# Kernel tuning notes

Measured on AMD Instinct MI355X. Metric: run time of the kernel, lower is better.

Reference implementation:

```python
import jax, jax.numpy as jnp
import numpy as np

LATENT_DIM = 32
INPUT_DIM = 16
N_UNITS = 20
N_TRAJ = 4096
T = 512


def setup_inputs() -> dict:
    key = jax.random.key(0)
    ks = jax.random.split(key, 8)
    cat_dim = LATENT_DIM + INPUT_DIM
    s1 = 1.0 / np.sqrt(cat_dim)
    s2 = 1.0 / np.sqrt(N_UNITS)
    return {
        "data": jax.random.normal(ks[0], (N_TRAJ, T, INPUT_DIM), dtype=jnp.float32),
        "time_steps": jnp.arange(T, dtype=jnp.float32),
        "Wu1": jax.random.normal(ks[1], (cat_dim, N_UNITS), dtype=jnp.float32) * s1,
        "bu1": jnp.zeros((N_UNITS,), dtype=jnp.float32),
        "Wu2": jax.random.normal(ks[2], (N_UNITS, LATENT_DIM), dtype=jnp.float32) * s2,
        "bu2": jnp.zeros((LATENT_DIM,), dtype=jnp.float32),
        "Wr1": jax.random.normal(ks[3], (cat_dim, N_UNITS), dtype=jnp.float32) * s1,
        "br1": jnp.zeros((N_UNITS,), dtype=jnp.float32),
        "Wr2": jax.random.normal(ks[4], (N_UNITS, LATENT_DIM), dtype=jnp.float32) * s2,
        "br2": jnp.zeros((LATENT_DIM,), dtype=jnp.float32),
        "Wn1": jax.random.normal(ks[5], (cat_dim, N_UNITS), dtype=jnp.float32) * s1,
        "bn1": jnp.zeros((N_UNITS,), dtype=jnp.float32),
        "Wn2": jax.random.normal(ks[6], (N_UNITS, LATENT_DIM), dtype=jnp.float32) * s2,
        "bn2": jnp.zeros((LATENT_DIM,), dtype=jnp.float32),
    }


def _mlp(h, W1, b1, W2, b2):
    # 2-layer MLP with tanh hidden, linear out
    return jnp.tanh(h @ W1 + b1) @ W2 + b2


def reference(data, time_steps, Wu1, bu1, Wu2, bu2, Wr1, br1, Wr2, br2, Wn1, bn1, Wn2, bn2):
    n_traj = data.shape[0]
    latent_dim = Wu2.shape[1]

    def step(prev_y, xi):
        yc = jnp.concatenate([prev_y, xi], axis=-1)            # [B, L+D]
        u = jax.nn.sigmoid(_mlp(yc, Wu1, bu1, Wu2, bu2))       # update gate
        r = jax.nn.sigmoid(_mlp(yc, Wr1, br1, Wr2, br2))       # reset gate
        cc = jnp.concatenate([prev_y * r, xi], axis=-1)
        n = jnp.tanh(_mlp(cc, Wn1, bn1, Wn2, bn2))             # candidate state
        new_y = (1.0 - u) * n + u * prev_y
        return new_y, new_y

    prev_y = jnp.zeros((n_traj, latent_dim), dtype=data.dtype)
    xs = jnp.swapaxes(data, 0, 1)                              # [T, B, D]
    yi, ys = jax.lax.scan(step, prev_y, xs)
    latent_ys = jnp.swapaxes(ys, 0, 1)                         # [B, T, L]
    return yi, latent_ys
```

## Files before the change

### kernel.cpp

```cpp
#include <hip/hip_runtime.h>

#define T_STEPS 512
#define NTRAJ   4096
#define LAT     32
#define INPD    16
#define HID     20
#define CAT     48

__device__ __forceinline__ float fast_tanh(float x) {
    float e = __expf(2.0f * x);
    float r = __builtin_amdgcn_rcpf(e + 1.0f);
    return fmaf(-2.0f, r, 1.0f);
}
__device__ __forceinline__ float fast_sigmoid(float x) {
    float e = __expf(-x);
    return __builtin_amdgcn_rcpf(e + 1.0f);
}

template<int I> __device__ __forceinline__ float ror16(float v) {
    if constexpr (I == 0) {
        return v;
    } else {
        int r = __builtin_amdgcn_update_dpp(0, __float_as_int(v),
                                            0x120 | I, 0xF, 0xF, true);
        return __int_as_float(r);
    }
}

#define REP16(M) M(0) M(1) M(2) M(3) M(4) M(5) M(6) M(7) \
                 M(8) M(9) M(10) M(11) M(12) M(13) M(14) M(15)

__global__ __launch_bounds__(256, 2) void rnn_fused(
    const float* __restrict__ data,
    const float* __restrict__ Wu1, const float* __restrict__ bu1,
    const float* __restrict__ Wu2, const float* __restrict__ bu2,
    const float* __restrict__ Wr1, const float* __restrict__ br1,
    const float* __restrict__ Wr2, const float* __restrict__ br2,
    const float* __restrict__ Wn1, const float* __restrict__ bn1,
    const float* __restrict__ Wn2, const float* __restrict__ bn2,
    float* __restrict__ out_yi, float* __restrict__ out_lat)
{
    const int tid  = threadIdx.x;
    const int w    = tid >> 6;
    const int lane = tid & 63;
    const int c    = lane & 31;
    const int g    = lane >> 5;
    const int p    = (lane >> 4) & 1;
    const int b    = (blockIdx.x << 2) + w;

    const float* W1 = g ? Wr1 : Wu1;
    const float* B1 = g ? br1 : bu1;
    const float* W2 = g ? Wr2 : Wu2;
    const float* B2 = g ? br2 : bu2;
    const bool realc = (c < HID);

    float wa_a[16], wa_b[16], wa_x[16], wb_a[16], wb_b[16];
    float wc_a[16], wc_b[16], wc_x[16], wd_a[16], wd_b[16];
    #pragma unroll
    for (int i = 0; i < 16; ++i) {
        int s  = (c - i) & 15;
        int sa = 16 * p + s;
        int sb = 16 * (1 - p) + s;
        int sx = 32 + s;
        wa_a[i] = realc ? W1[sa * HID + c] : 0.0f;
        wa_b[i] = realc ? W1[sb * HID + c] : 0.0f;
        wa_x[i] = realc ? W1[sx * HID + c] : 0.0f;
        wb_a[i] = (sa < HID) ? W2[sa * LAT + c] : 0.0f;
        wb_b[i] = (sb < HID) ? W2[sb * LAT + c] : 0.0f;
        wc_a[i] = realc ? Wn1[sa * HID + c] : 0.0f;
        wc_b[i] = realc ? Wn1[sb * HID + c] : 0.0f;
        wc_x[i] = realc ? Wn1[sx * HID + c] : 0.0f;
        wd_a[i] = (sa < HID) ? Wn2[sa * LAT + c] : 0.0f;
        wd_b[i] = (sb < HID) ? Wn2[sb * LAT + c] : 0.0f;
    }
    const float ba = realc ? B1[c] : 0.0f;
    const float bb = B2[c];
    const float bc = realc ? bn1[c] : 0.0f;
    const float bd = bn2[c];

    const float* xptr = data + (size_t)b * T_STEPS * INPD + (lane & 15);
    float x0 = xptr[0];
    float x1 = xptr[INPD];

    float y  = 0.0f;
    float y2 = 0.0f;
    float* olat = out_lat + (size_t)b * T_STEPS * LAT + c;

    for (int t = 0; t < T_STEPS; ++t) {
        int tf = t + 2; tf = (tf < T_STEPS) ? tf : (T_STEPS - 1);
        float xn = xptr[(size_t)tf * INPD];

        float acc[4] = {ba, 0.f, 0.f, 0.f};
        #define PA(i) \
            acc[(i)&3]     = fmaf(ror16<(i)>(y),  wa_a[(i)], acc[(i)&3]); \
            acc[((i)+1)&3] = fmaf(ror16<(i)>(y2), wa_b[(i)], acc[((i)+1)&3]); \
            acc[((i)+2)&3] = fmaf(ror16<(i)>(x0), wa_x[(i)], acc[((i)+2)&3]);
        REP16(PA)
        #undef PA
        float h1 = fast_tanh((acc[0] + acc[1]) + (acc[2] + acc[3]));
        float h2 = __shfl_xor(h1, 16);

        float bcc[4] = {bb, 0.f, 0.f, 0.f};
        #define PB(i) \
            bcc[(i)&3]     = fmaf(ror16<(i)>(h1), wb_a[(i)], bcc[(i)&3]); \
            bcc[((i)+1)&3] = fmaf(ror16<(i)>(h2), wb_b[(i)], bcc[((i)+1)&3]);
        REP16(PB)
        #undef PB
        float gate = fast_sigmoid((bcc[0] + bcc[1]) + (bcc[2] + bcc[3]));

        float exch  = __shfl_xor(gate, 32);
        float u_all = g ? exch : gate;
        float r_all = g ? gate : exch;
        float ry    = r_all * y;
        float ry2   = __shfl_xor(ry, 16);

        float ccc[4] = {bc, 0.f, 0.f, 0.f};
        #define PC(i) \
            ccc[(i)&3]     = fmaf(ror16<(i)>(ry),  wc_a[(i)], ccc[(i)&3]); \
            ccc[((i)+1)&3] = fmaf(ror16<(i)>(ry2), wc_b[(i)], ccc[((i)+1)&3]); \
            ccc[((i)+2)&3] = fmaf(ror16<(i)>(x0),  wc_x[(i)], ccc[((i)+2)&3]);
        REP16(PC)
        #undef PC
        float hn  = fast_tanh((ccc[0] + ccc[1]) + (ccc[2] + ccc[3]));
        float hn2 = __shfl_xor(hn, 16);

        float dcc[4] = {bd, 0.f, 0.f, 0.f};
        #define PD(i) \
            dcc[(i)&3]     = fmaf(ror16<(i)>(hn),  wd_a[(i)], dcc[(i)&3]); \
            dcc[((i)+1)&3] = fmaf(ror16<(i)>(hn2), wd_b[(i)], dcc[((i)+1)&3]);
        REP16(PD)
        #undef PD
        float n = fast_tanh((dcc[0] + dcc[1]) + (dcc[2] + dcc[3]));

        float ny = fmaf(u_all, y - n, n);
        y  = ny;
        y2 = __shfl_xor(ny, 16);
        if (lane < 32) olat[(size_t)t * LAT] = ny;

        x0 = x1; x1 = xn;
    }

    if (lane < 32) out_yi[(size_t)b * LAT + c] = y;
}

extern "C" void kernel_launch(void* const* d_in, const int* in_sizes, int n_in,
                              void* d_out, int out_size, void* d_ws, size_t ws_size,
                              hipStream_t stream) {
    const float* data = (const float*)d_in[0];
    const float* Wu1 = (const float*)d_in[2];
    const float* bu1 = (const float*)d_in[3];
    const float* Wu2 = (const float*)d_in[4];
    const float* bu2 = (const float*)d_in[5];
    const float* Wr1 = (const float*)d_in[6];
    const float* br1 = (const float*)d_in[7];
    const float* Wr2 = (const float*)d_in[8];
    const float* br2 = (const float*)d_in[9];
    const float* Wn1 = (const float*)d_in[10];
    const float* bn1 = (const float*)d_in[11];
    const float* Wn2 = (const float*)d_in[12];
    const float* bn2 = (const float*)d_in[13];

    float* out_yi  = (float*)d_out;
    float* out_lat = out_yi + (size_t)NTRAJ * LAT;

    rnn_fused<<<NTRAJ / 4, 256, 0, stream>>>(
        data, Wu1, bu1, Wu2, bu2, Wr1, br1, Wr2, br2, Wn1, bn1, Wn2, bn2,
        out_yi, out_lat);
}
```

Before: 1.123 ms.

## Interleave two trajectories per wavefront to hide serial dependency latency

Each 64-lane wavefront now processes two independent trajectories in an interleaved way, so the dependent FMA/DPP/shuffle chains of one trajectory can overlap with those of the other. Blocks shrink to a single wave (2048 blocks of 64 threads), and the DPP rotate switches from update_dpp with old=0 to mov_dpp without bound_ctrl. This trades fewer total waves and possibly higher register pressure for more instruction-level parallelism within each wave.

```diff
diff --git a/kernel.cpp b/kernel.cpp
--- a/kernel.cpp
+++ b/kernel.cpp
@@ -21,16 +21,35 @@
     if constexpr (I == 0) {
         return v;
     } else {
-        int r = __builtin_amdgcn_update_dpp(0, __float_as_int(v),
-                                            0x120 | I, 0xF, 0xF, true);
-        return __int_as_float(r);
-    }
-}
-
-#define REP16(M) M(0) M(1) M(2) M(3) M(4) M(5) M(6) M(7) \
-                 M(8) M(9) M(10) M(11) M(12) M(13) M(14) M(15)
-
-__global__ __launch_bounds__(256, 2) void rnn_fused(
+        return __int_as_float(__builtin_amdgcn_mov_dpp(
+            __float_as_int(v), 0x120 | I, 0xF, 0xF, false));
+    }
+}
+
+#define MPA(i, ACC, Y, Y2, X) \
+    ACC[(i)&3]     = fmaf(ror16<(i)>(Y),  wa_a[(i)], ACC[(i)&3]); \
+    ACC[((i)+1)&3] = fmaf(ror16<(i)>(Y2), wa_b[(i)], ACC[((i)+1)&3]); \
+    ACC[((i)+2)&3] = fmaf(ror16<(i)>(X),  wa_x[(i)], ACC[((i)+2)&3]);
+#define MPB(i, ACC, H, H2, X) \
+    ACC[(i)&3]     = fmaf(ror16<(i)>(H),  wb_a[(i)], ACC[(i)&3]); \
+    ACC[((i)+1)&3] = fmaf(ror16<(i)>(H2), wb_b[(i)], ACC[((i)+1)&3]);
+#define MPC(i, ACC, RY, RY2, X) \
+    ACC[(i)&3]     = fmaf(ror16<(i)>(RY),  wc_a[(i)], ACC[(i)&3]); \
+    ACC[((i)+1)&3] = fmaf(ror16<(i)>(RY2), wc_b[(i)], ACC[((i)+1)&3]); \
+    ACC[((i)+2)&3] = fmaf(ror16<(i)>(X),   wc_x[(i)], ACC[((i)+2)&3]);
+#define MPD(i, ACC, HN, HN2, X) \
+    ACC[(i)&3]     = fmaf(ror16<(i)>(HN),  wd_a[(i)], ACC[(i)&3]); \
+    ACC[((i)+1)&3] = fmaf(ror16<(i)>(HN2), wd_b[(i)], ACC[((i)+1)&3]);
+
+#define REP16(M, ACC, S1, S2, S3) \
+    M(0,ACC,S1,S2,S3)  M(1,ACC,S1,S2,S3)  M(2,ACC,S1,S2,S3)  M(3,ACC,S1,S2,S3) \
+    M(4,ACC,S1,S2,S3)  M(5,ACC,S1,S2,S3)  M(6,ACC,S1,S2,S3)  M(7,ACC,S1,S2,S3) \
+    M(8,ACC,S1,S2,S3)  M(9,ACC,S1,S2,S3)  M(10,ACC,S1,S2,S3) M(11,ACC,S1,S2,S3) \
+    M(12,ACC,S1,S2,S3) M(13,ACC,S1,S2,S3) M(14,ACC,S1,S2,S3) M(15,ACC,S1,S2,S3)
+
+#define RED4(A) ((A[0] + A[1]) + (A[2] + A[3]))
+
+__global__ __launch_bounds__(64, 1) void rnn_fused(
     const float* __restrict__ data,
     const float* __restrict__ Wu1, const float* __restrict__ bu1,
     const float* __restrict__ Wu2, const float* __restrict__ bu2,
@@ -40,13 +59,12 @@
     const float* __restrict__ Wn2, const float* __restrict__ bn2,
     float* __restrict__ out_yi, float* __restrict__ out_lat)
 {
-    const int tid  = threadIdx.x;
-    const int w    = tid >> 6;
-    const int lane = tid & 63;
+    const int lane = threadIdx.x & 63;
     const int c    = lane & 31;
     const int g    = lane >> 5;
     const int p    = (lane >> 4) & 1;
-    const int b    = (blockIdx.x << 2) + w;
+    const int bA   = blockIdx.x * 2;
+    const int bB   = bA + 1;
 
     const float* W1 = g ? Wr1 : Wu1;
     const float* B1 = g ? br1 : bu1;
@@ -78,69 +96,82 @@
     const float bc = realc ? bn1[c] : 0.0f;
     const float bd = bn2[c];
 
-    const float* xptr = data + (size_t)b * T_STEPS * INPD + (lane & 15);
-    float x0 = xptr[0];
-    float x1 = xptr[INPD];
-
-    float y  = 0.0f;
-    float y2 = 0.0f;
-    float* olat = out_lat + (size_t)b * T_STEPS * LAT + c;
+    const float* xpA = data + (size_t)bA * T_STEPS * INPD + (lane & 15);
+    const float* xpB = data + (size_t)bB * T_STEPS * INPD + (lane & 15);
+    float x0A = xpA[0],    x0B = xpB[0];
+    float x1A = xpA[INPD], x1B = xpB[INPD];
+
+    float yA = 0.0f, y2A = 0.0f;
+    float yB = 0.0f, y2B = 0.0f;
+    float* olA = out_lat + (size_t)bA * T_STEPS * LAT + c;
+    float* olB = out_lat + (size_t)bB * T_STEPS * LAT + c;
 
     for (int t = 0; t < T_STEPS; ++t) {
         int tf = t + 2; tf = (tf < T_STEPS) ? tf : (T_STEPS - 1);
-        float xn = xptr[(size_t)tf * INPD];
-
-        float acc[4] = {ba, 0.f, 0.f, 0.f};
-        #define PA(i) \
-            acc[(i)&3]     = fmaf(ror16<(i)>(y),  wa_a[(i)], acc[(i)&3]); \
-            acc[((i)+1)&3] = fmaf(ror16<(i)>(y2), wa_b[(i)], acc[((i)+1)&3]); \
-            acc[((i)+2)&3] = fmaf(ror16<(i)>(x0), wa_x[(i)], acc[((i)+2)&3]);
-        REP16(PA)
-        #undef PA
-        float h1 = fast_tanh((acc[0] + acc[1]) + (acc[2] + acc[3]));
-        float h2 = __shfl_xor(h1, 16);
-
-        float bcc[4] = {bb, 0.f, 0.f, 0.f};
-        #define PB(i) \
-            bcc[(i)&3]     = fmaf(ror16<(i)>(h1), wb_a[(i)], bcc[(i)&3]); \
-            bcc[((i)+1)&3] = fmaf(ror16<(i)>(h2), wb_b[(i)], bcc[((i)+1)&3]);
-        REP16(PB)
-        #undef PB
-        float gate = fast_sigmoid((bcc[0] + bcc[1]) + (bcc[2] + bcc[3]));
-
-        float exch  = __shfl_xor(gate, 32);
-        float u_all = g ? exch : gate;
-        float r_all = g ? gate : exch;
-        float ry    = r_all * y;
-        float ry2   = __shfl_xor(ry, 16);
-
-        float ccc[4] = {bc, 0.f, 0.f, 0.f};
-        #define PC(i) \
-            ccc[(i)&3]     = fmaf(ror16<(i)>(ry),  wc_a[(i)], ccc[(i)&3]); \
-            ccc[((i)+1)&3] = fmaf(ror16<(i)>(ry2), wc_b[(i)], ccc[((i)+1)&3]); \
-            ccc[((i)+2)&3] = fmaf(ror16<(i)>(x0),  wc_x[(i)], ccc[((i)+2)&3]);
-        REP16(PC)
-        #undef PC
-        float hn  = fast_tanh((ccc[0] + ccc[1]) + (ccc[2] + ccc[3]));
-        float hn2 = __shfl_xor(hn, 16);
-
-        float dcc[4] = {bd, 0.f, 0.f, 0.f};
-        #define PD(i) \
-            dcc[(i)&3]     = fmaf(ror16<(i)>(hn),  wd_a[(i)], dcc[(i)&3]); \
-            dcc[((i)+1)&3] = fmaf(ror16<(i)>(hn2), wd_b[(i)], dcc[((i)+1)&3]);
-        REP16(PD)
-        #undef PD
-        float n = fast_tanh((dcc[0] + dcc[1]) + (dcc[2] + dcc[3]));
-
-        float ny = fmaf(u_all, y - n, n);
-        y  = ny;
-        y2 = __shfl_xor(ny, 16);
-        if (lane < 32) olat[(size_t)t * LAT] = ny;
-
-        x0 = x1; x1 = xn;
-    }
-
-    if (lane < 32) out_yi[(size_t)b * LAT + c] = y;
+        float xnA = xpA[(size_t)tf * INPD];
+        float xnB = xpB[(size_t)tf * INPD];
+
+        float aA[4] = {ba, 0.f, 0.f, 0.f};
+        float aB[4] = {ba, 0.f, 0.f, 0.f};
+        REP16(MPA, aA, yA, y2A, x0A)
+        REP16(MPA, aB, yB, y2B, x0B)
+        float h1A = fast_tanh(RED4(aA));
+        float h1B = fast_tanh(RED4(aB));
+        float h2A = __shfl_xor(h1A, 16);
+        float h2B = __shfl_xor(h1B, 16);
+
+        float bqA[4] = {bb, 0.f, 0.f, 0.f};
+        float bqB[4] = {bb, 0.f, 0.f, 0.f};
+        REP16(MPB, bqA, h1A, h2A, 0)
+        REP16(MPB, bqB, h1B, h2B, 0)
+        float gateA = fast_sigmoid(RED4(bqA));
+        float gateB = fast_sigmoid(RED4(bqB));
+
+        float exchA = __shfl_xor(gateA, 32);
+        float exchB = __shfl_xor(gateB, 32);
+        float uA = g ? exchA : gateA;
+        float uB = g ? exchB : gateB;
+        float rA = g ? gateA : exchA;
+        float rB = g ? gateB : exchB;
+        float ryA = rA * yA;
+        float ryB = rB * yB;
+        float ry2A = __shfl_xor(ryA, 16);
+        float ry2B = __shfl_xor(ryB, 16);
+
+        float cqA[4] = {bc, 0.f, 0.f, 0.f};
+        float cqB[4] = {bc, 0.f, 0.f, 0.f};
+        REP16(MPC, cqA, ryA, ry2A, x0A)
+        REP16(MPC, cqB, ryB, ry2B, x0B)
+        float hnA = fast_tanh(RED4(cqA));
+        float hnB = fast_tanh(RED4(cqB));
+        float hn2A = __shfl_xor(hnA, 16);
+        float hn2B = __shfl_xor(hnB, 16);
+
+        float dqA[4] = {bd, 0.f, 0.f, 0.f};
+        float dqB[4] = {bd, 0.f, 0.f, 0.f};
+        REP16(MPD, dqA, hnA, hn2A, 0)
+        REP16(MPD, dqB, hnB, hn2B, 0)
+        float nA = fast_tanh(RED4(dqA));
+        float nB = fast_tanh(RED4(dqB));
+
+        float nyA = fmaf(uA, yA - nA, nA);
+        float nyB = fmaf(uB, yB - nB, nB);
+        yA = nyA; yB = nyB;
+        y2A = __shfl_xor(nyA, 16);
+        y2B = __shfl_xor(nyB, 16);
+        if (lane < 32) {
+            olA[(size_t)t * LAT] = nyA;
+            olB[(size_t)t * LAT] = nyB;
+        }
+
+        x0A = x1A; x1A = xnA;
+        x0B = x1B; x1B = xnB;
+    }
+
+    if (lane < 32) {
+        out_yi[(size_t)bA * LAT + c] = yA;
+        out_yi[(size_t)bB * LAT + c] = yB;
+    }
 }
 
 extern "C" void kernel_launch(void* const* d_in, const int* in_sizes, int n_in,
@@ -163,7 +194,7 @@
     float* out_yi  = (float*)d_out;
     float* out_lat = out_yi + (size_t)NTRAJ * LAT;
 
-    rnn_fused<<<NTRAJ / 4, 256, 0, stream>>>(
+    rnn_fused<<<NTRAJ / 2, 64, 0, stream>>>(
         data, Wu1, bu1, Wu2, bu2, Wr1, br1, Wr2, br2, Wn1, bn1, Wn2, bn2,
         out_yi, out_lat);
 }
```

After: 1.391 ms. 1.24x slower.
